# Optimization experiments

Hardware: AMD Instinct MI355X
Metric: run time of the kernel (lower is better)

Reference implementation:

```python
import jax, jax.numpy as jnp
import numpy as np

B, L, H, N, CH = 8, 2048, 512, 64, 1


def setup_inputs() -> dict:
    key = jax.random.key(0)
    ks = jax.random.split(key, 7)
    # S4D-Lin style init: w = -0.5 + i*pi*n, with slight noise on the real part
    w_re = -(0.5 + 0.1 * jax.random.uniform(ks[0], (H, N), dtype=jnp.float32))
    w_im = jnp.broadcast_to(jnp.pi * jnp.arange(N, dtype=jnp.float32), (H, N)).copy()
    C_re = jax.random.normal(ks[1], (CH, H, N), dtype=jnp.float32)
    C_im = jax.random.normal(ks[2], (CH, H, N), dtype=jnp.float32)
    D = jax.random.normal(ks[3], (CH, H), dtype=jnp.float32)
    # log-uniform dt in [1e-3, 1e-1]
    log_dt = jax.random.uniform(ks[4], (H,), dtype=jnp.float32,
                                minval=jnp.log(1e-3), maxval=jnp.log(1e-1))
    dt = jnp.exp(log_dt)
    u = jax.random.normal(ks[5], (B, L, H), dtype=jnp.float32)
    return {"u": u, "w_re": w_re, "w_im": w_im, "C_re": C_re,
            "C_im": C_im, "D": D, "dt": dt}


def reference(u, w_re, w_im, C_re, C_im, D, dt):
    # u: [B, L, H] -> [B, H, L]
    uT = jnp.swapaxes(u, -1, -2)
    l = uT.shape[-1]
    h = dt.shape[-1]
    w = (w_re + 1j * w_im).astype(jnp.complex64)          # [t, n]
    v = h // w.shape[0]
    w = jnp.tile(w, (v, 1))                                # [h, n]
    C = (C_re + 1j * C_im).astype(jnp.complex64)           # [c, h, n]
    # --- kernel generation ---
    dtA = w * dt[:, None]                                  # [h, n]
    K = jnp.arange(l) * dtA[..., None]                     # [h, n, l]
    Cs = C * ((jnp.exp(dtA) - 1.0) / w)                    # [c, h, n]
    k = 2.0 * jnp.einsum('chn,hnl->chl', Cs, jnp.exp(K)).real  # [c, h, l]
    # --- FFT convolution ---
    k_f = jnp.fft.rfft(k, n=2 * l - 1)                     # [c, h, l]
    u_f = jnp.fft.rfft(uT, n=2 * l - 1)                    # [B, h, l]
    y_f = jnp.einsum('...hl,chl->...chl', u_f, k_f)        # [B, c, h, l]
    y = jnp.fft.irfft(y_f, n=2 * l)[..., :l]               # [B, c, h, l]
    # skip connection
    y = y + jnp.einsum('...hl,ch->...chl', uT, D)
    # '... c h l -> ... l c h'
    return jnp.moveaxis(y, (-3, -2, -1), (-2, -1, -3))
```

## Files before the change

kernel.cpp:

```cpp
#include <hip/hip_runtime.h>
#include <hip/hip_bf16.h>
#include <math.h>


namespace {
constexpr int cB = 8;
constexpr int cL = 2048;
constexpr int cH = 512;
constexpr int cN = 64;
constexpr int M1 = 4095;
constexpr int M2 = 4096;
constexpr int BH = cB * cH;
constexpr int MA = BH + cH;

constexpr size_t S0   = 2 * ((size_t)cH * cN * 6);
constexpr size_t S_B1 = S0;
constexpr size_t S_A  = S_B1 + (size_t)4096 * 2048;
constexpr size_t S_T2 = S_A  + (size_t)MA * 2048;
constexpr size_t S_U  = S_T2 + (size_t)2048 * 4096;
constexpr size_t S_AP = S_B1;
}

typedef __attribute__((ext_vector_type(8))) short short8;
typedef __attribute__((ext_vector_type(4))) short sh4;
typedef __attribute__((ext_vector_type(4))) float f32x4;

static __device__ inline short f2bf(float x) {
    __hip_bfloat16 h = __float2bfloat16(x);
    return *reinterpret_cast<short*>(&h);
}
static __device__ inline float bf2f(short s) {
    return __uint_as_float(((unsigned int)(unsigned short)s) << 16);
}
static __device__ __forceinline__ void load_lds16(const short* g, short* l) {
    __builtin_amdgcn_global_load_lds(
        (const __attribute__((address_space(1))) void*)g,
        (__attribute__((address_space(3))) void*)l, 16, 0, 0);
}
#define WAIT_LGKM0() do { asm volatile("s_waitcnt lgkmcnt(0)" ::: "memory"); \
                          __builtin_amdgcn_sched_barrier(0); } while (0)
#define WAIT_VM(n)   do { asm volatile("s_waitcnt vmcnt(" #n ")" ::: "memory"); \
                          __builtin_amdgcn_sched_barrier(0); } while (0)
#define BAR() __builtin_amdgcn_s_barrier()

__global__ __launch_bounds__(256) void k_tabs(short* __restrict__ Wb)
{
    int tid = threadIdx.x;
    if (blockIdx.x < 2048) {
        int j  = blockIdx.x;
        int t0 = tid * 8;
        int p0 = (int)(((long)j * t0) % M1);
        float c, s, cs, ss;
        sincosf((6.283185307179586f / (float)M1) * (float)p0, &s, &c);
        sincosf((6.283185307179586f / (float)M1) * (float)j,  &ss, &cs);
        short8 vc, vs;
#pragma unroll
        for (int i = 0; i < 8; ++i) {
            vc[i] = f2bf(c); vs[i] = f2bf(s);
            float tr = c * cs - s * ss;
            s = c * ss + s * cs;
            c = tr;
        }
        *(short8*)&Wb[S_B1 + (size_t)(2 * j)     * 2048 + t0] = vc;
        *(short8*)&Wb[S_B1 + (size_t)(2 * j + 1) * 2048 + t0] = vs;
    } else {
        int r   = blockIdx.x - 2048;
        int p   = r >> 10, tau = r & 1023;
        int t   = 2 * tau + p;
        int k0  = tid * 8;
        float stepang = (6.283185307179586f / (float)M2) * (float)t;
        float cs, ss; sincosf(stepang, &ss, &cs);
        short8 v;
        if (k0 < 1024) {
            int ph = (k0 * t) & (M2 - 1);
            float c, s; sincosf((6.283185307179586f / (float)M2) * (float)ph, &s, &c);
#pragma unroll
            for (int i = 0; i < 8; ++i) {
                v[i] = f2bf(c);
                float tr = c * cs - s * ss;
                s = c * ss + s * cs;
                c = tr;
            }
        } else {
            int j0 = k0 - 1023;
            int ph = (j0 * t) & (M2 - 1);
            float c, s; sincosf((6.283185307179586f / (float)M2) * (float)ph, &s, &c);
#pragma unroll
            for (int i = 0; i < 8; ++i) {
                int k = k0 + i;
                v[i] = (k == 2047) ? f2bf((tau & 1) ? -1.f : 1.f) : f2bf(s);
                float tr = c * cs - s * ss;
                s = c * ss + s * cs;
                c = tr;
            }
        }
        *(short8*)&Wb[S_T2 + (size_t)r * 2048 + k0] = v;
    }
}

__global__ __launch_bounds__(256) void k_trans(const float* __restrict__ u,
                                               short* __restrict__ Wb)
{
    __shared__ float tile[64][65];
    int t0 = blockIdx.x * 64;
    int h0 = blockIdx.y * 64;
    int b  = blockIdx.z;
    int cx = threadIdx.x & 63, r0 = threadIdx.x >> 6;
#pragma unroll
    for (int i = 0; i < 16; ++i) {
        int row = r0 + i * 4;
        tile[row][cx] = u[((size_t)b * cL + t0 + row) * cH + h0 + cx];
    }
    __syncthreads();
    short* A = Wb + S_A;
#pragma unroll
    for (int i = 0; i < 16; ++i) {
        int hrow = r0 + i * 4;
        A[(size_t)(b * cH + h0 + hrow) * 2048 + t0 + cx] = f2bf(tile[cx][hrow]);
    }
}

__global__ __launch_bounds__(256) void k_kgen(
    const float* __restrict__ w_re, const float* __restrict__ w_im,
    const float* __restrict__ C_re, const float* __restrict__ C_im,
    const float* __restrict__ dt, short* __restrict__ Wb)
{
    __shared__ float md[cN * 6];
    int h = blockIdx.x, tid = threadIdx.x;
    if (tid < cN) {
        int idx = h * cN + tid;
        double dtv = dt[h];
        double wr = w_re[idx], wi = w_im[idx];
        double ar = wr * dtv, ai = wi * dtv;
        double er = exp(ar);
        double zs, zc; sincos(ai, &zs, &zc);
        double zr = er * zc, zi = er * zs;
        double nr = zr - 1.0, ni = zi;
        double inv = 1.0 / (wr * wr + wi * wi);
        double gr = (nr * wr + ni * wi) * inv;
        double gi = (ni * wr - nr * wi) * inv;
        double cr = C_re[idx], ci = C_im[idx];
        md[tid*6+0] = (float)(cr * gr - ci * gi);
        md[tid*6+1] = (float)(cr * gi + ci * gr);
        md[tid*6+2] = (float)zr; md[tid*6+3] = (float)zi;
        md[tid*6+4] = (float)ar; md[tid*6+5] = (float)ai;
    }
    __syncthreads();
    int t0 = tid * 8;
    float acc[8] = {0.f, 0.f, 0.f, 0.f, 0.f, 0.f, 0.f, 0.f};
    for (int n = 0; n < cN; ++n) {
        float csr = md[n*6+0], csi = md[n*6+1];
        float zr  = md[n*6+2], zi  = md[n*6+3];
        float ar  = md[n*6+4], ai  = md[n*6+5];
        float mag = expf(ar * (float)t0);
        double ph = fmod((double)ai * (double)t0, 6.283185307179586);
        float s, c; sincosf((float)ph, &s, &c);
        float pr = mag * c, pi = mag * s;
#pragma unroll
        for (int i = 0; i < 8; ++i) {
            acc[i] += csr * pr - csi * pi;
            float tr = pr * zr - pi * zi;
            pi = pr * zi + pi * zr;
            pr = tr;
        }
    }
    short8 v;
#pragma unroll
    for (int i = 0; i < 8; ++i) v[i] = f2bf(2.f * acc[i]);
    *reinterpret_cast<short8*>(&Wb[S_A + (size_t)(BH + h) * 2048 + t0]) = v;
}

#define MFMA16(AR, BR, ACC) \
    _Pragma("unroll") for (int kk = 0; kk < 2; ++kk) \
    _Pragma("unroll") for (int ni = 0; ni < 2; ++ni) \
    _Pragma("unroll") for (int mi = 0; mi < 4; ++mi) \
        ACC[mi][ni] = __builtin_amdgcn_mfma_f32_16x16x32_bf16(AR[mi][kk], BR[ni][kk], ACC[mi][ni], 0, 0, 0);

__device__ __forceinline__ void gemm8p_core(
    const short* __restrict__ Ag, int lda,
    const short* __restrict__ Bg, int ldb,
    int m0, int n0, int nt, short* lds, f32x4 (&acc)[4][4][2])
{
    const int tid  = threadIdx.x;
    const int wave = tid >> 6, lane = tid & 63;
    const int wm = wave >> 2, wn = wave & 3;
    const int lm = lane & 15, lk = lane >> 4;
    const int srow8 = lane >> 3;
    const int scol  = (lane & 7) * 8;

    auto stage = [&](const short* G, int ldg, int row0, int half, int kt, int sb) {
        short* l0 = lds + sb + (size_t)((kt & 1) * 2 + half) * 8192;
#pragma unroll
        for (int q = 0; q < 2; ++q) {
            int chunk = wave * 2 + q;
            int r = chunk * 8 + srow8;
            int c = scol ^ ((r & 7) << 3);
            load_lds16(G + (size_t)(row0 + half * 128 + r) * ldg + kt * 64 + c,
                       l0 + chunk * 512);
        }
    };
    auto rdA = [&](int qa, int kt, int mi, int kk) -> short8 {
        int rl = wm * 64 + mi * 16 + lm;
        int c  = (kk * 32 + lk * 8) ^ ((rl & 7) << 3);
        return *(const short8*)(lds + (size_t)((kt & 1) * 2 + qa) * 8192 + rl * 64 + c);
    };
    auto rdB = [&](int qb, int kt, int ni, int kk) -> short8 {
        int rl = wn * 32 + ni * 16 + lm;
        int c  = (kk * 32 + lk * 8) ^ ((rl & 7) << 3);
        return *(const short8*)(lds + 32768 + (size_t)((kt & 1) * 2 + qb) * 8192 + rl * 64 + c);
    };

    stage(Ag, lda, m0, 0, 0, 0);
    stage(Bg, ldb, n0, 0, 0, 32768);
    stage(Bg, ldb, n0, 1, 0, 32768);
    stage(Ag, lda, m0, 1, 0, 0);
    stage(Ag, lda, m0, 0, 1, 0);
    stage(Bg, ldb, n0, 0, 1, 32768);
    stage(Bg, ldb, n0, 1, 1, 32768);
    stage(Ag, lda, m0, 1, 1, 0);
    WAIT_VM(12);
    BAR();

    short8 a0[4][2], a1[4][2], b0[2][2], b1[2][2];
    for (int t = 0; t < nt; ++t) {
        const bool st = (t + 2 < nt);
#pragma unroll
        for (int mi = 0; mi < 4; ++mi) { a0[mi][0] = rdA(0, t, mi, 0); a0[mi][1] = rdA(0, t, mi, 1); }
#pragma unroll
        for (int ni = 0; ni < 2; ++ni) { b0[ni][0] = rdB(0, t, ni, 0); b0[ni][1] = rdB(0, t, ni, 1); }
        BAR();
        WAIT_LGKM0();
        __builtin_amdgcn_s_setprio(1);
        MFMA16(a0, b0, acc[0]);
        __builtin_amdgcn_s_setprio(0);
        if (st) { WAIT_VM(10); } else { WAIT_VM(0); }
        BAR();
#pragma unroll
        for (int ni = 0; ni < 2; ++ni) { b1[ni][0] = rdB(1, t, ni, 0); b1[ni][1] = rdB(1, t, ni, 1); }
        if (st) { stage(Ag, lda, m0, 0, t + 2, 0); stage(Bg, ldb, n0, 0, t + 2, 32768); }
        BAR();
        WAIT_LGKM0();
        __builtin_amdgcn_s_setprio(1);
        MFMA16(a0, b1, acc[1]);
        __builtin_amdgcn_s_setprio(0);
        if (st) { WAIT_VM(12); } else { WAIT_VM(0); }
        BAR();
#pragma unroll
        for (int mi = 0; mi < 4; ++mi) { a1[mi][0] = rdA(1, t, mi, 0); a1[mi][1] = rdA(1, t, mi, 1); }
        if (st) stage(Bg, ldb, n0, 1, t + 2, 32768);
        BAR();
        WAIT_LGKM0();
        __builtin_amdgcn_s_setprio(1);
        MFMA16(a1, b1, acc[3]);
        __builtin_amdgcn_s_setprio(0);
        BAR();
        if (st) stage(Ag, lda, m0, 1, t + 2, 0);
        __builtin_amdgcn_s_setprio(1);
        MFMA16(a1, b0, acc[2]);
        __builtin_amdgcn_s_setprio(0);
        if (st) { WAIT_VM(12); } else { WAIT_VM(0); }
        BAR();
    }
}

__global__ __launch_bounds__(512, 2) void k_fwd8(short* __restrict__ Wb)
{
    __shared__ short lds_s[65536];
    int tile = (blockIdx.x & 7) * 32 + (blockIdx.x >> 3);
    const int m0 = (tile >> 4) * 256, n0 = (tile & 15) * 256;
    const int tid = threadIdx.x;
    const int wave = tid >> 6, lane = tid & 63;
    const int wm = wave >> 2, wn = wave & 3;
    const int lm = lane & 15, lk = lane >> 4;

    f32x4 acc[4][4][2] = {};
    gemm8p_core(Wb + S_A, 2048, Wb + S_B1, 2048, m0, n0, 32, lds_s, acc);

    short* Ys = Wb + S_U;
    const short* KF = Wb + S_U;
    short (*M)[136] = (short(*)[136])lds_s;
    for (int q = 0; q < 4; ++q) {
        __syncthreads();
#pragma unroll
        for (int mi = 0; mi < 4; ++mi)
#pragma unroll
        for (int ni = 0; ni < 2; ++ni)
#pragma unroll
        for (int r = 0; r < 4; ++r)
            M[wm * 64 + mi * 16 + lk * 4 + r][wn * 32 + ni * 16 + lm] =
                f2bf(acc[q][mi][ni][r]);
        __syncthreads();
        const int jwin = (n0 >> 1) + (q & 1) * 64;
#pragma unroll
        for (int pass = 0; pass < 4; ++pass) {
            int rl = pass * 32 + (tid >> 4);
            int p0 = (tid & 15) * 4;
            int rowg = m0 + (q >> 1) * 128 + rl;
            int h = rowg & (cH - 1);
            short8 kf8 = *(const short8*)&KF[(size_t)(4096 + h) * 4096 + 2 * (jwin + p0)];
            short8 m8  = *(const short8*)&M[rl][2 * p0];
            sh4 yr4, yi4;
#pragma unroll
            for (int i = 0; i < 4; ++i) {
                float C  = bf2f(m8[2*i]),  S  = bf2f(m8[2*i+1]);
                float Ck = bf2f(kf8[2*i]), Sk = bf2f(kf8[2*i+1]);
                int j = jwin + p0 + i;
                float sc = (j == 0 ? 1.0f : 2.0f) * (1.0f / (float)M2);
                yr4[i] = f2bf(sc * (Ck * C - Sk * S));
                yi4[i] = f2bf(sc * (Ck * S + Sk * C));
            }
            *(sh4*)&Ys[(size_t)rowg * 4096 + jwin + p0]        = yr4;
            *(sh4*)&Ys[(size_t)rowg * 4096 + 2048 + jwin + p0] = yi4;
        }
    }
}

__global__ __launch_bounds__(256, 2) void k_kfg(short* __restrict__ Wb)
{
    __shared__ __align__(16) short As[128][32];
    __shared__ __align__(16) short Bs[128][32];
    const short* A = Wb + S_A;
    const short* B = Wb + S_B1;
    short* U = Wb + S_U;
    const int tid = threadIdx.x;
    const int m0 = 4096 + blockIdx.y * 128, n0 = blockIdx.x * 128;
    const int wave = tid >> 6, lane = tid & 63;
    const int wr = wave >> 1, wc = wave & 1;
    const int lm = lane & 15, lk = lane >> 4;
    const int srow = lane >> 2, scol = (lane & 3) * 8;

    f32x4 acc[4][4] = {};
    for (int k0 = 0; k0 < 2048; k0 += 32) {
        __syncthreads();
        {
            int c0 = wave * 2;
            load_lds16(&A[(size_t)(m0 + c0*16      + srow)*2048 + k0 + scol], &As[c0*16][0]);
            load_lds16(&A[(size_t)(m0 + c0*16 + 16 + srow)*2048 + k0 + scol], &As[c0*16+16][0]);
            load_lds16(&B[(size_t)(n0 + c0*16      + srow)*2048 + k0 + scol], &Bs[c0*16][0]);
            load_lds16(&B[(size_t)(n0 + c0*16 + 16 + srow)*2048 + k0 + scol], &Bs[c0*16+16][0]);
        }
        __syncthreads();
        short8 a[4];
#pragma unroll
        for (int mi = 0; mi < 4; ++mi)
            a[mi] = *(const short8*)&As[wr*64 + mi*16 + lm][lk*8];
#pragma unroll
        for (int ni = 0; ni < 4; ++ni) {
            short8 b = *(const short8*)&Bs[wc*64 + ni*16 + lm][lk*8];
#pragma unroll
            for (int mi = 0; mi < 4; ++mi)
                acc[mi][ni] = __builtin_amdgcn_mfma_f32_16x16x32_bf16(a[mi], b, acc[mi][ni], 0, 0, 0);
        }
    }
#pragma unroll
    for (int mi = 0; mi < 4; ++mi)
#pragma unroll
    for (int ni = 0; ni < 4; ++ni)
#pragma unroll
    for (int r = 0; r < 4; ++r) {
        int row = m0 + wr*64 + mi*16 + lk*4 + r;
        int col = n0 + wc*64 + ni*16 + lm;
        U[(size_t)row * 4096 + col] = f2bf(acc[mi][ni][r]);
    }
}

__global__ __launch_bounds__(256) void k_par(short* __restrict__ Wb)
{
    __shared__ short row[4096];
    int bh = blockIdx.x, tid = threadIdx.x;
    const short* Ysr = Wb + S_U + (size_t)bh * 4096;
    *(short8*)&row[tid * 16]     = *(const short8*)&Ysr[tid * 16];
    *(short8*)&row[tid * 16 + 8] = *(const short8*)&Ysr[tid * 16 + 8];
    __syncthreads();
    short* Ae = Wb + S_AP + (size_t)bh * 2048;
    short* Ao = Wb + S_AP + (size_t)(4096 + bh) * 2048;
    int k0 = tid * 8;
    short8 ve, vo;
#pragma unroll
    for (int i = 0; i < 8; ++i) {
        int k = k0 + i;
        float e, o;
        if (k == 0) {
            e = o = bf2f(row[0]);
        } else if (k < 1024) {
            float a = bf2f(row[k]), b = bf2f(row[2048 - k]);
            e = a + b; o = a - b;
        } else if (k < 2047) {
            int j = k - 1023;
            float a = bf2f(row[2048 + j]), b = bf2f(row[4096 - j]);
            e = a - b; o = a + b;
        } else {
            e = bf2f(row[1024]);
            o = bf2f(row[2048 + 1024]);
        }
        ve[i] = f2bf(e); vo[i] = f2bf(o);
    }
    *(short8*)&Ae[k0] = ve;
    *(short8*)&Ao[k0] = vo;
}

__global__ __launch_bounds__(512, 1) void k_invB(const float* __restrict__ u,
                                                 const float* __restrict__ Dp,
                                                 short* __restrict__ Wb,
                                                 float* __restrict__ out)
{
    __shared__ short lds_s[57344];
    int tile = (blockIdx.x & 7) * 32 + (blockIdx.x >> 3);
    const int m0   = (tile >> 4) * 256;
    const int rest = tile & 15;
    const int p    = rest >> 3;
    const int n0   = (rest & 7) * 128;
    const int tid = threadIdx.x;
    const int wave = tid >> 6, lane = tid & 63;
    const int wm = wave >> 2, wn = wave & 3;
    const int lm = lane & 15, lk = lane >> 4;
    const int srow8 = lane >> 3;
    const int scol  = (lane & 7) * 8;
    constexpr int nt = 32;
    short* lds = lds_s;
    const short* Ag = Wb + S_AP + (size_t)p * 4096 * 2048;
    const short* Bg = Wb + S_T2 + (size_t)p * 1024 * 2048;

    auto stageA = [&](int half, int kt) {
        short* l0 = lds + (size_t)((kt & 1) * 2 + half) * 8192;
#pragma unroll
        for (int q = 0; q < 2; ++q) {
            int chunk = wave * 2 + q;
            int r = chunk * 8 + srow8;
            int c = scol ^ ((r & 7) << 3);
            load_lds16(Ag + (size_t)(m0 + half * 128 + r) * 2048 + kt * 64 + c,
                       l0 + chunk * 512);
        }
    };
    auto stageB = [&](int kt, int slot) {
        short* l0 = lds + 32768 + (size_t)slot * 8192;
#pragma unroll
        for (int q = 0; q < 2; ++q) {
            int chunk = wave * 2 + q;
            int r = chunk * 8 + srow8;
            int c = scol ^ ((r & 7) << 3);
            load_lds16(Bg + (size_t)(n0 + r) * 2048 + kt * 64 + c,
                       l0 + chunk * 512);
        }
    };
    auto rdA = [&](int half, int kt, int mi, int kk) -> short8 {
        int rl = wm * 64 + mi * 16 + lm;
        int c  = (kk * 32 + lk * 8) ^ ((rl & 7) << 3);
        return *(const short8*)(lds + (size_t)((kt & 1) * 2 + half) * 8192 + rl * 64 + c);
    };
    auto rdB = [&](int slot, int ni, int kk) -> short8 {
        int rl = wn * 32 + ni * 16 + lm;
        int c  = (kk * 32 + lk * 8) ^ ((rl & 7) << 3);
        return *(const short8*)(lds + 32768 + (size_t)slot * 8192 + rl * 64 + c);
    };

    f32x4 acc[2][4][2] = {};

    stageA(0, 0);
    stageB(0, 0);
    stageA(1, 0);
    stageA(0, 1);
    stageB(1, 1);
    stageB(2, 2);
    WAIT_VM(6);
    BAR();

    short8 a[4][2], b[2][2];
    int bs = 0;
    for (int t = 0; t < nt; ++t) {
        const bool deep = (t + 3 < nt);
#pragma unroll
        for (int mi = 0; mi < 4; ++mi) { a[mi][0] = rdA(0, t, mi, 0); a[mi][1] = rdA(0, t, mi, 1); }
#pragma unroll
        for (int ni = 0; ni < 2; ++ni) { b[ni][0] = rdB(bs, ni, 0); b[ni][1] = rdB(bs, ni, 1); }
        if (t + 1 < nt) stageA(1, t + 1);
        BAR();
        WAIT_LGKM0();
        __builtin_amdgcn_s_setprio(1);
        MFMA16(a, b, acc[0]);
        __builtin_amdgcn_s_setprio(0);
        if (deep) { WAIT_VM(6); } else { WAIT_VM(0); }
        BAR();
#pragma unroll
        for (int mi = 0; mi < 4; ++mi) { a[mi][0] = rdA(1, t, mi, 0); a[mi][1] = rdA(1, t, mi, 1); }
        if (t + 2 < nt) stageA(0, t + 2);
        if (t + 3 < nt) stageB(t + 3, bs);
        BAR();
        WAIT_LGKM0();
        __builtin_amdgcn_s_setprio(1);
        MFMA16(a, b, acc[1]);
        __builtin_amdgcn_s_setprio(0);
        if (deep) { WAIT_VM(6); } else { WAIT_VM(0); }
        BAR();
        bs = (bs == 2) ? 0 : bs + 1;
    }

    const int b_  = m0 >> 9;
    const int h00 = m0 & 511;
    float (*T)[132] = (float(*)[132])lds_s;
#pragma unroll
    for (int q = 0; q < 2; ++q) {
        __syncthreads();
#pragma unroll
        for (int mi = 0; mi < 4; ++mi)
#pragma unroll
        for (int ni = 0; ni < 2; ++ni) {
            int tl = wn * 32 + ni * 16 + lm;
            int hl = wm * 64 + mi * 16 + lk * 4;
            *(float4*)&T[tl][hl] = *(float4*)&acc[q][mi][ni];
        }
        __syncthreads();
        int hg = h00 + q * 128 + (tid & 31) * 4;
        float4 dv = *(const float4*)&Dp[hg];
#pragma unroll
        for (int it = 0; it < 8; ++it) {
            int tl = (tid >> 5) + it * 16;
            int tg = 2 * (n0 + tl) + p;
            size_t gidx = ((size_t)b_ * cL + tg) * cH + hg;
            float4 uv = *(const float4*)&u[gidx];
            float4 yv = *(float4*)&T[tl][(tid & 31) * 4];
            yv.x += dv.x * uv.x;
            yv.y += dv.y * uv.y;
            yv.z += dv.z * uv.z;
            yv.w += dv.w * uv.w;
            *(float4*)&out[gidx] = yv;
        }
    }
}

extern "C" void kernel_launch(void* const* d_in, const int* in_sizes, int n_in,
                              void* d_out, int out_size, void* d_ws, size_t ws_size,
                              hipStream_t stream) {
    const float* u    = (const float*)d_in[0];
    const float* w_re = (const float*)d_in[1];
    const float* w_im = (const float*)d_in[2];
    const float* C_re = (const float*)d_in[3];
    const float* C_im = (const float*)d_in[4];
    const float* Dp   = (const float*)d_in[5];
    const float* dt   = (const float*)d_in[6];
    float* out = (float*)d_out;
    short* Wb  = (short*)d_ws;

    hipLaunchKernelGGL(k_tabs,  dim3(4096), dim3(256), 0, stream, Wb);
    hipLaunchKernelGGL(k_trans, dim3(cL / 64, cH / 64, cB), dim3(256), 0, stream, u, Wb);
    hipLaunchKernelGGL(k_kgen,  dim3(cH), dim3(256), 0, stream,
                       w_re, w_im, C_re, C_im, dt, Wb);
    hipLaunchKernelGGL(k_kfg,   dim3(32, 4), dim3(256), 0, stream, Wb);
    hipLaunchKernelGGL(k_fwd8,  dim3(256), dim3(512), 0, stream, Wb);
    hipLaunchKernelGGL(k_par,   dim3(BH), dim3(256), 0, stream, Wb);
    hipLaunchKernelGGL(k_invB,  dim3(256), dim3(512), 0, stream, u, Dp, Wb, out);
}
```

Before: 212.6 us.

## Fuse even/odd parity split into forward GEMM epilogue, drop k_par kernel

```diff
diff --git a/kernel.cpp b/kernel.cpp
--- a/kernel.cpp
+++ b/kernel.cpp
@@ -18,11 +18,10 @@
 constexpr size_t S_A  = S_B1 + (size_t)4096 * 2048;
 constexpr size_t S_T2 = S_A  + (size_t)MA * 2048;
 constexpr size_t S_U  = S_T2 + (size_t)2048 * 4096;
-constexpr size_t S_AP = S_B1;
 }
 
 typedef __attribute__((ext_vector_type(8))) short short8;
-typedef __attribute__((ext_vector_type(4))) short sh4;
+typedef __attribute__((ext_vector_type(2))) short sh2;
 typedef __attribute__((ext_vector_type(4))) float f32x4;
 
 static __device__ inline short f2bf(float x) {
@@ -48,6 +47,7 @@
     int tid = threadIdx.x;
     if (blockIdx.x < 2048) {
         int j  = blockIdx.x;
+        int base = (j < 1024) ? 4 * j : (j == 1024 ? 2 : 4 * (2048 - j) + 2);
         int t0 = tid * 8;
         int p0 = (int)(((long)j * t0) % M1);
         float c, s, cs, ss;
@@ -61,8 +61,8 @@
             s = c * ss + s * cs;
             c = tr;
         }
-        *(short8*)&Wb[S_B1 + (size_t)(2 * j)     * 2048 + t0] = vc;
-        *(short8*)&Wb[S_B1 + (size_t)(2 * j + 1) * 2048 + t0] = vs;
+        *(short8*)&Wb[S_B1 + (size_t)base       * 2048 + t0] = vc;
+        *(short8*)&Wb[S_B1 + (size_t)(base + 1) * 2048 + t0] = vs;
     } else {
         int r   = blockIdx.x - 2048;
         int p   = r >> 10, tau = r & 1023;
@@ -82,13 +82,13 @@
                 c = tr;
             }
         } else {
-            int j0 = k0 - 1023;
+            int j0 = k0 - 1024;
             int ph = (j0 * t) & (M2 - 1);
             float c, s; sincosf((6.283185307179586f / (float)M2) * (float)ph, &s, &c);
 #pragma unroll
             for (int i = 0; i < 8; ++i) {
                 int k = k0 + i;
-                v[i] = (k == 2047) ? f2bf((tau & 1) ? -1.f : 1.f) : f2bf(s);
+                v[i] = (k == 1024) ? f2bf((tau & 1) ? -1.f : 1.f) : f2bf(s);
                 float tr = c * cs - s * ss;
                 s = c * ss + s * cs;
                 c = tr;
@@ -276,7 +276,7 @@
     f32x4 acc[4][4][2] = {};
     gemm8p_core(Wb + S_A, 2048, Wb + S_B1, 2048, m0, n0, 32, lds_s, acc);
 
-    short* Ys = Wb + S_U;
+    short* Uw = Wb + S_U;
     const short* KF = Wb + S_U;
     short (*M)[136] = (short(*)[136])lds_s;
     for (int q = 0; q < 4; ++q) {
@@ -290,27 +290,42 @@
             M[wm * 64 + mi * 16 + lk * 4 + r][wn * 32 + ni * 16 + lm] =
                 f2bf(acc[q][mi][ni][r]);
         __syncthreads();
-        const int jwin = (n0 >> 1) + (q & 1) * 64;
+        const int pq0 = (n0 >> 2) + (q & 1) * 32;
 #pragma unroll
         for (int pass = 0; pass < 4; ++pass) {
             int rl = pass * 32 + (tid >> 4);
-            int p0 = (tid & 15) * 4;
+            int cp = (tid & 15) * 2;
             int rowg = m0 + (q >> 1) * 128 + rl;
             int h = rowg & (cH - 1);
-            short8 kf8 = *(const short8*)&KF[(size_t)(4096 + h) * 4096 + 2 * (jwin + p0)];
-            short8 m8  = *(const short8*)&M[rl][2 * p0];
-            sh4 yr4, yi4;
-#pragma unroll
-            for (int i = 0; i < 4; ++i) {
-                float C  = bf2f(m8[2*i]),  S  = bf2f(m8[2*i+1]);
-                float Ck = bf2f(kf8[2*i]), Sk = bf2f(kf8[2*i+1]);
-                int j = jwin + p0 + i;
-                float sc = (j == 0 ? 1.0f : 2.0f) * (1.0f / (float)M2);
-                yr4[i] = f2bf(sc * (Ck * C - Sk * S));
-                yi4[i] = f2bf(sc * (Ck * S + Sk * C));
+            int colg = n0 + (q & 1) * 128 + cp * 4;
+            short8 kf8 = *(const short8*)&KF[(size_t)(4096 + h) * 4096 + colg];
+            short8 m8  = *(const short8*)&M[rl][cp * 4];
+            sh2 vce, vco, vse, vso;
+#pragma unroll
+            for (int i = 0; i < 2; ++i) {
+                float C  = bf2f(m8[4*i]),   S  = bf2f(m8[4*i+1]);
+                float C2 = bf2f(m8[4*i+2]), S2 = bf2f(m8[4*i+3]);
+                float Ck  = bf2f(kf8[4*i]),   Sk  = bf2f(kf8[4*i+1]);
+                float Ck2 = bf2f(kf8[4*i+2]), Sk2 = bf2f(kf8[4*i+3]);
+                int p = pq0 + cp + i;
+                float scp = (p == 0 ? 1.0f : 2.0f) * (1.0f / (float)M2);
+                float scq = 2.0f / (float)M2;
+                float yrp = scp * (Ck * C - Sk * S);
+                float yip = scp * (Ck * S + Sk * C);
+                float yrq = scq * (Ck2 * C2 - Sk2 * S2);
+                float yiq = scq * (Ck2 * S2 + Sk2 * C2);
+                float ce, co, se, so;
+                if (p == 0) { ce = yrp; co = yrp; se = yrq; so = yiq; }
+                else { ce = yrp + yrq; co = yrp - yrq; se = yip - yiq; so = yip + yiq; }
+                vce[i] = f2bf(ce); vco[i] = f2bf(co);
+                vse[i] = f2bf(se); vso[i] = f2bf(so);
             }
-            *(sh4*)&Ys[(size_t)rowg * 4096 + jwin + p0]        = yr4;
-            *(sh4*)&Ys[(size_t)rowg * 4096 + 2048 + jwin + p0] = yi4;
+            size_t base = (size_t)rowg * 4096;
+            int kx = pq0 + cp;
+            *(sh2*)&Uw[base + kx]        = vce;
+            *(sh2*)&Uw[base + 1024 + kx] = vse;
+            *(sh2*)&Uw[base + 2048 + kx] = vco;
+            *(sh2*)&Uw[base + 3072 + kx] = vso;
         }
     }
 }
@@ -362,41 +377,6 @@
         int col = n0 + wc*64 + ni*16 + lm;
         U[(size_t)row * 4096 + col] = f2bf(acc[mi][ni][r]);
     }
-}
-
-__global__ __launch_bounds__(256) void k_par(short* __restrict__ Wb)
-{
-    __shared__ short row[4096];
-    int bh = blockIdx.x, tid = threadIdx.x;
-    const short* Ysr = Wb + S_U + (size_t)bh * 4096;
-    *(short8*)&row[tid * 16]     = *(const short8*)&Ysr[tid * 16];
-    *(short8*)&row[tid * 16 + 8] = *(const short8*)&Ysr[tid * 16 + 8];
-    __syncthreads();
-    short* Ae = Wb + S_AP + (size_t)bh * 2048;
-    short* Ao = Wb + S_AP + (size_t)(4096 + bh) * 2048;
-    int k0 = tid * 8;
-    short8 ve, vo;
-#pragma unroll
-    for (int i = 0; i < 8; ++i) {
-        int k = k0 + i;
-        float e, o;
-        if (k == 0) {
-            e = o = bf2f(row[0]);
-        } else if (k < 1024) {
-            float a = bf2f(row[k]), b = bf2f(row[2048 - k]);
-            e = a + b; o = a - b;
-        } else if (k < 2047) {
-            int j = k - 1023;
-            float a = bf2f(row[2048 + j]), b = bf2f(row[4096 - j]);
-            e = a - b; o = a + b;
-        } else {
-            e = bf2f(row[1024]);
-            o = bf2f(row[2048 + 1024]);
-        }
-        ve[i] = f2bf(e); vo[i] = f2bf(o);
-    }
-    *(short8*)&Ae[k0] = ve;
-    *(short8*)&Ao[k0] = vo;
 }
 
 __global__ __launch_bounds__(512, 1) void k_invB(const float* __restrict__ u,
@@ -418,7 +398,7 @@
     const int scol  = (lane & 7) * 8;
     constexpr int nt = 32;
     short* lds = lds_s;
-    const short* Ag = Wb + S_AP + (size_t)p * 4096 * 2048;
+    const short* Ag = Wb + S_U + (size_t)p * 2048;
     const short* Bg = Wb + S_T2 + (size_t)p * 1024 * 2048;
 
     auto stageA = [&](int half, int kt) {
@@ -428,7 +408,7 @@
             int chunk = wave * 2 + q;
             int r = chunk * 8 + srow8;
             int c = scol ^ ((r & 7) << 3);
-            load_lds16(Ag + (size_t)(m0 + half * 128 + r) * 2048 + kt * 64 + c,
+            load_lds16(Ag + (size_t)(m0 + half * 128 + r) * 4096 + kt * 64 + c,
                        l0 + chunk * 512);
         }
     };
@@ -547,6 +527,5 @@
                        w_re, w_im, C_re, C_im, dt, Wb);
     hipLaunchKernelGGL(k_kfg,   dim3(32, 4), dim3(256), 0, stream, Wb);
     hipLaunchKernelGGL(k_fwd8,  dim3(256), dim3(512), 0, stream, Wb);
-    hipLaunchKernelGGL(k_par,   dim3(BH), dim3(256), 0, stream, Wb);
     hipLaunchKernelGGL(k_invB,  dim3(256), dim3(512), 0, stream, u, Dp, Wb, out);
 }
```

Measured after the change: 202.9 us. 4.5% less time.
